# Optimization experiments

Hardware: AMD Instinct MI355X
Metric: run time of the kernel (lower is better)

The kernel has to match this reference:

```python
import jax, jax.numpy as jnp
import numpy as np

B, M, N, D, H = 8, 64, 64, 256, 8

def setup_inputs() -> dict:
    key = jax.random.key(0)
    kx, kq, kk, kv, ko = jax.random.split(key, 5)
    x = jax.random.normal(kx, (B, M, N, D), dtype=jnp.float32)
    q = jax.random.normal(kq, (H, D, D), dtype=jnp.float32)
    k = jax.random.normal(kk, (D, D), dtype=jnp.float32)
    v = jax.random.normal(kv, (D, D), dtype=jnp.float32)
    o = jax.random.normal(ko, (H, D, D), dtype=jnp.float32)
    return {"x": x, "q": q, "k": k, "v": v, "o": o}

def reference(x, q, k, v, o):
    # x: [b,m,n,d]; q,o: [h,d,d]; k,v: [d,d]
    Q = jnp.einsum('bmnd,hdk->bhmnk', x, q)      # [b,h,m,n,d]
    h_half = Q.shape[1] // 2
    Q1, Q2 = Q[:, :h_half], Q[:, h_half:]
    K = jnp.einsum('bmnd,dk->bmnk', x, k)        # [b,m,n,d]
    V = jnp.einsum('bmnd,dv->bmnv', x, v)        # [b,m,n,d]

    # Axis 1: attend along the m (row) axis for each column y
    logits1 = jnp.einsum('bhxyk,bzyk->bhyxz', Q1, K)   # [b,h/2,n,m,m]
    scores1 = jax.nn.softmax(logits1, axis=-1)
    O1 = jnp.einsum('bhyxz,bzyv->bhxyv', scores1, V)   # [b,h/2,m,n,d]

    # Axis 2: attend along the n (column) axis for each row x
    logits2 = jnp.einsum('bhxyk,bxzk->bhxyz', Q2, K)   # [b,h/2,m,n,n]
    scores2 = jax.nn.softmax(logits2, axis=-1)
    O2 = jnp.einsum('bhxyz,bxzv->bhxyv', scores2, V)   # [b,h/2,m,n,d]

    O = jnp.concatenate([O1, O2], axis=1)              # [b,h,m,n,d]
    # Faithful to original: 'bhmnd,hdv->bmnd' keeps d, sums over h and v
    Z = jnp.einsum('bhmnd,hdv->bmnd', O, o)
    return Z
```

## Files before the change

### kernel.cpp

```cpp
#include <hip/hip_runtime.h>

typedef unsigned short u16;
typedef __attribute__((ext_vector_type(8))) short short8;
typedef __attribute__((ext_vector_type(4))) float f32x4;

__device__ __forceinline__ float bf2f(u16 u){ return __uint_as_float(((unsigned)u)<<16); }
__device__ __forceinline__ u16 f2bf(float f){
  unsigned u = __float_as_uint(f);
  unsigned r = u + 0x7fffu + ((u>>16)&1u);
  return (u16)(r>>16);
}

#define MFMA16(a,b,c) __builtin_amdgcn_mfma_f32_16x16x32_bf16(a,b,c,0,0,0)

static constexpr int XS_STR  = 264;
static constexpr int PS_STR  = 72;
static constexpr int WT_STR  = 72;
static constexpr int XHI_OFF = 0;
static constexpr int XLO_OFF = 16896;
static constexpr int GT_OFF  = 33792;
static constexpr int XVT_OFF = 50688;
static constexpr int PS_OFF  = 69120;
static constexpr int SMRE_OFF= 73728;
static constexpr int SMEM_BYTES = (73728 + 512)*2;

static constexpr int MH_SMEM = 70656*2;


__global__ void prep_kernel(const float* __restrict__ k, const float* __restrict__ v,
                            const float* __restrict__ o, u16* __restrict__ khi,
                            u16* __restrict__ klo, u16* __restrict__ vT,
                            float* __restrict__ soP, float4* __restrict__ outz){
  __shared__ float Ts[64*65];
  const int blk = blockIdx.x, tid = threadIdx.x;
  if (blk < 64){
    int base = blk*1024 + tid*4;
    const float4 f4 = *(const float4*)(k + base);
    ushort4 hv, lv;
    hv.x=f2bf(f4.x); lv.x=f2bf(f4.x-bf2f(hv.x));
    hv.y=f2bf(f4.y); lv.y=f2bf(f4.y-bf2f(hv.y));
    hv.z=f2bf(f4.z); lv.z=f2bf(f4.z-bf2f(hv.z));
    hv.w=f2bf(f4.w); lv.w=f2bf(f4.w-bf2f(hv.w));
    *(ushort4*)&khi[base] = hv;
    *(ushort4*)&klo[base] = lv;
  } else if (blk < 80){
    int t = blk - 64;
    const int bi = (t>>2)<<6, bj = (t&3)<<6;
    #pragma unroll
    for (int p=0;p<4;p++){
      int idx4 = tid + (p<<8);
      int i = idx4 >> 4, c4 = (idx4 & 15) << 2;
      const float4 f4 = *(const float4*)(v + ((bi+i)<<8) + bj + c4);
      Ts[i*65+c4]=f4.x; Ts[i*65+c4+1]=f4.y; Ts[i*65+c4+2]=f4.z; Ts[i*65+c4+3]=f4.w;
    }
    __syncthreads();
    #pragma unroll
    for (int p=0;p<2;p++){
      int ch = tid + (p<<8);
      int j = ch >> 3, i8 = (ch & 7) << 3;
      short8 t8;
      #pragma unroll
      for (int e=0;e<8;e++) t8[e] = (short)f2bf(Ts[(i8+e)*65 + j]);
      *(short8*)&vT[((bj+j)<<8) + bi + i8] = t8;
    }
  } else if (blk < 336){
    int p = blk - 80;
    int h = p >> 5, base = (p & 31) << 3;
    int w = tid >> 6, l = tid & 63;
    #pragma unroll
    for (int i=0;i<2;i++){
      int row = base + w*2 + i;
      const float4 f4 = *(const float4*)(o + (((h<<8)+row)<<8) + (l<<2));
      float s = f4.x + f4.y + f4.z + f4.w;
      #pragma unroll
      for (int off=32; off>=1; off>>=1) s += __shfl_xor(s, off, 64);
      if (l==0) soP[(h<<8)+row] = s;
    }
  } else {
    int z = blk - 336;
    const float4 zf4 = {0.f,0.f,0.f,0.f};
    #pragma unroll
    for (int i=0;i<16;i++) outz[z*4096 + i*256 + tid] = zf4;
  }
}

__global__ __launch_bounds__(256,1) void mh_kernel(
    const float* __restrict__ q, const u16* __restrict__ khi,
    const u16* __restrict__ klo, u16* __restrict__ mhi, u16* __restrict__ mlo)
{
  extern __shared__ u16 sm[];
  u16* Qhi = sm;
  u16* Qlo = sm + 16896;
  u16* Chi = sm + 33792;
  u16* Clo = sm + 52224;

  const int tid = threadIdx.x;
  const int w = tid >> 6, lane = tid & 63;
  const int quad = lane >> 4, m16 = lane & 15;
  const int cw = w << 6, koq = quad << 3;
  const int h = blockIdx.x >> 2, dt = (blockIdx.x & 3) << 6;

  #pragma unroll
  for (int i=0;i<16;i++){
    int idx4 = i*256 + tid;
    int tr = idx4 >> 6, c4 = (idx4 & 63) << 2;
    const float4 xv = *(const float4*)(q + (((h<<8)+dt+tr)<<8) + c4);
    ushort4 hv, lv;
    hv.x=f2bf(xv.x); lv.x=f2bf(xv.x-bf2f(hv.x));
    hv.y=f2bf(xv.y); lv.y=f2bf(xv.y-bf2f(hv.y));
    hv.z=f2bf(xv.z); lv.z=f2bf(xv.z-bf2f(hv.z));
    hv.w=f2bf(xv.w); lv.w=f2bf(xv.w-bf2f(hv.w));
    *(ushort4*)&Qhi[tr*XS_STR + c4] = hv;
    *(ushort4*)&Qlo[tr*XS_STR + c4] = lv;
  }
  __syncthreads();

  const f32x4 zf = {0.f,0.f,0.f,0.f};
  f32x4 acc[4][4];
  #pragma unroll
  for (int r=0;r<4;r++)
    #pragma unroll
    for (int c=0;c<4;c++) acc[r][c] = zf;

  short8 Bh[2][4], Bl[2][4];
  #pragma unroll
  for (int c=0;c<4;c++){
    Bh[0][c] = *(const short8*)&khi[(cw + c*16 + m16)*256 + koq];
    Bl[0][c] = *(const short8*)&klo[(cw + c*16 + m16)*256 + koq];
  }
  #pragma unroll
  for (int kk=0;kk<8;kk++){
    const int cur = kk&1, nxt = cur^1;
    if (kk<7){
      const int ko2 = ((kk+1)<<5) + koq;
      #pragma unroll
      for (int c=0;c<4;c++){
        Bh[nxt][c] = *(const short8*)&khi[(cw + c*16 + m16)*256 + ko2];
        Bl[nxt][c] = *(const short8*)&klo[(cw + c*16 + m16)*256 + ko2];
      }
    }
    const int ko = (kk<<5) + koq;
    short8 Ah[4], Al[4];
    #pragma unroll
    for (int r=0;r<4;r++) Ah[r] = *(const short8*)&Qhi[(r*16+m16)*XS_STR + ko];
    #pragma unroll
    for (int r=0;r<4;r++) Al[r] = *(const short8*)&Qlo[(r*16+m16)*XS_STR + ko];
    #pragma unroll
    for (int r=0;r<4;r++)
      #pragma unroll
      for (int c=0;c<4;c++){
        acc[r][c] = MFMA16(Ah[r], Bh[cur][c], acc[r][c]);
        acc[r][c] = MFMA16(Ah[r], Bl[cur][c], acc[r][c]);
        acc[r][c] = MFMA16(Al[r], Bh[cur][c], acc[r][c]);
      }
  }

  #pragma unroll
  for (int r=0;r<4;r++)
    #pragma unroll
    for (int c=0;c<4;c++)
      #pragma unroll
      for (int g=0; g<4; g++){
        int drow = r*16 + quad*4 + g;
        int dp   = cw + c*16 + m16;
        float vv = acc[r][c][g];
        u16 hh = f2bf(vv);
        Chi[dp*WT_STR + drow] = hh;
        Clo[dp*WT_STR + drow] = f2bf(vv - bf2f(hh));
      }
  __syncthreads();

  #pragma unroll
  for (int p=0;p<8;p++){
    int ch = tid + (p<<8);
    int dp = ch >> 3, i8 = (ch & 7) << 3;
    *(int4*)&mhi[(((h<<8)+dp)<<8) + dt + i8] = *(const int4*)&Chi[dp*WT_STR + i8];
    *(int4*)&mlo[(((h<<8)+dp)<<8) + dt + i8] = *(const int4*)&Clo[dp*WT_STR + i8];
  }
}

__global__ __launch_bounds__(512,2) void attn_kernel(
    const float* __restrict__ x, const u16* __restrict__ mhiP,
    const u16* __restrict__ mloP, const u16* __restrict__ vT,
    const float* __restrict__ soP, float* __restrict__ out)
{
  extern __shared__ u16 sm[];
  u16* Xhi = sm + XHI_OFF;
  u16* Xlo = sm + XLO_OFF;
  u16* Gt  = sm + GT_OFF;
  u16* Xvt = sm + XVT_OFF;
  u16* Ps  = sm + PS_OFF;
  float* SMf = (float*)(sm + SMRE_OFF);

  const int tid  = threadIdx.x;
  const int w    = tid >> 6, lane = tid & 63;
  const int quad = lane >> 4, m16 = lane & 15;
  const int br   = blockIdx.x >> 9;
  const int idx  = blockIdx.x & 511;
  const int b    = idx >> 6, s = idx & 63;
  const int cw   = w << 5;
  const int rs   = (w >> 1) << 4;
  const int zh   = w & 1;
  const int koq  = quad << 3;

  auto tok = [&](int t)->int {
    int m = br ? s : t;
    int n = br ? t : s;
    return (((b<<6) + m) << 14) + (n << 8);
  };

  #pragma unroll
  for (int i=0;i<8;i++){
    int idx4 = i*512 + tid;
    int tr = idx4 >> 6, c4 = (idx4 & 63) << 2;
    const float4 xv = *(const float4*)(x + tok(tr) + c4);
    ushort4 hv, lv;
    hv.x=f2bf(xv.x); lv.x=f2bf(xv.x-bf2f(hv.x));
    hv.y=f2bf(xv.y); lv.y=f2bf(xv.y-bf2f(hv.y));
    hv.z=f2bf(xv.z); lv.z=f2bf(xv.z-bf2f(hv.z));
    hv.w=f2bf(xv.w); lv.w=f2bf(xv.w-bf2f(hv.w));
    *(ushort4*)&Xhi[tr*XS_STR + c4] = hv;
    *(ushort4*)&Xlo[tr*XS_STR + c4] = lv;
  }
  __syncthreads();

  short8 XB[16];
  #pragma unroll
  for (int kk=0;kk<8;kk++)
    #pragma unroll
    for (int c=0;c<2;c++)
      XB[kk*2+c] = *(const short8*)&Xhi[((zh<<5) + c*16 + m16)*XS_STR + (kk<<5) + koq];

  const f32x4 zf = {0.f,0.f,0.f,0.f};
  f32x4 acc[4][2];

  auto mm3 = [&](const u16* __restrict__ Whi, const u16* __restrict__ Wlo){
    #pragma unroll
    for (int r=0;r<4;r++){ acc[r][0] = zf; acc[r][1] = zf; }
    short8 Bh[2][2], Bl[2][2];
    #pragma unroll
    for (int c=0;c<2;c++){
      Bh[0][c] = *(const short8*)&Whi[(cw + c*16 + m16)*256 + koq];
      Bl[0][c] = *(const short8*)&Wlo[(cw + c*16 + m16)*256 + koq];
    }
    #pragma unroll
    for (int kk=0;kk<8;kk++){
      const int cur = kk&1, nxt = cur^1;
      if (kk<7){
        const int ko2 = ((kk+1)<<5) + koq;
        #pragma unroll
        for (int c=0;c<2;c++){
          Bh[nxt][c] = *(const short8*)&Whi[(cw + c*16 + m16)*256 + ko2];
          Bl[nxt][c] = *(const short8*)&Wlo[(cw + c*16 + m16)*256 + ko2];
        }
      }
      const int ko = (kk<<5) + koq;
      short8 Ah[4], Al[4];
      #pragma unroll
      for (int r=0;r<4;r++) Ah[r] = *(const short8*)&Xhi[(r*16+m16)*XS_STR + ko];
      #pragma unroll
      for (int r=0;r<4;r++) Al[r] = *(const short8*)&Xlo[(r*16+m16)*XS_STR + ko];
      #pragma unroll
      for (int r=0;r<4;r++)
        #pragma unroll
        for (int c=0;c<2;c++){
          acc[r][c] = MFMA16(Ah[r], Bh[cur][c], acc[r][c]);
          acc[r][c] = MFMA16(Ah[r], Bl[cur][c], acc[r][c]);
          acc[r][c] = MFMA16(Al[r], Bh[cur][c], acc[r][c]);
        }
    }
  };

  {
    #pragma unroll
    for (int r=0;r<4;r++){ acc[r][0] = zf; acc[r][1] = zf; }
    #pragma unroll
    for (int kk=0;kk<8;kk++){
      const int ko = (kk<<5) + koq;
      short8 A[4], Bf[2];
      #pragma unroll
      for (int r=0;r<4;r++) A[r]  = *(const short8*)&Xhi[(r*16+m16)*XS_STR + ko];
      #pragma unroll
      for (int c=0;c<2;c++) Bf[c] = *(const short8*)&vT[(cw + c*16 + m16)*256 + ko];
      #pragma unroll
      for (int r=0;r<4;r++)
        #pragma unroll
        for (int c=0;c<2;c++) acc[r][c] = MFMA16(A[r], Bf[c], acc[r][c]);
    }
    #pragma unroll
    for (int r=0;r<4;r++)
      #pragma unroll
      for (int c=0;c<2;c++)
        #pragma unroll
        for (int g=0; g<4; g++){
          int z  = r*16 + quad*4 + g;
          int vc = cw + c*16 + m16;
          Xvt[vc*WT_STR + z] = f2bf(acc[r][c][g]);
        }
  }

  f32x4 Z[4][2];
  #pragma unroll
  for (int r=0;r<4;r++){ Z[r][0] = zf; Z[r][1] = zf; }

  for (int h=0; h<4; h++){
    const int gh = br*4 + h;

    mm3(mhiP + gh*65536, mloP + gh*65536);
    #pragma unroll
    for (int r=0;r<4;r++)
      #pragma unroll
      for (int c=0;c<2;c++)
        #pragma unroll
        for (int g=0; g<4; g++){
          int row = r*16 + quad*4 + g;
          int col = cw + c*16 + m16;
          Gt[row*XS_STR + col] = f2bf(acc[r][c][g]);
        }
    __syncthreads();

    f32x4 L[2];
    L[0] = zf; L[1] = zf;
    #pragma unroll
    for (int kk=0;kk<8;kk++){
      const int ko = (kk<<5) + koq;
      short8 A = *(const short8*)&Gt[(rs+m16)*XS_STR + ko];
      #pragma unroll
      for (int c=0;c<2;c++){
        L[c] = MFMA16(A, XB[kk*2+c], L[c]);
        short8 Bl = *(const short8*)&Xlo[((zh<<5) + c*16 + m16)*XS_STR + ko];
        L[c] = MFMA16(A, Bl, L[c]);
      }
    }
    __syncthreads();
    #pragma unroll
    for (int r=0;r<4;r++)
      #pragma unroll
      for (int c=0;c<2;c++)
        #pragma unroll
        for (int g=0; g<4; g++){
          int row = r*16 + quad*4 + g;
          int col = cw + c*16 + m16;
          float vv = acc[r][c][g];
          u16 hh = f2bf(vv);
          Gt[row*XS_STR + col] = f2bf(vv - bf2f(hh));
        }
    __syncthreads();

    #pragma unroll
    for (int kk=0;kk<8;kk++){
      const int ko = (kk<<5) + koq;
      short8 A = *(const short8*)&Gt[(rs+m16)*XS_STR + ko];
      #pragma unroll
      for (int c=0;c<2;c++)
        L[c] = MFMA16(A, XB[kk*2+c], L[c]);
    }

    float mxl[4], sml[4];
    #pragma unroll
    for (int g=0; g<4; g++){
      float mx = fmaxf(L[0][g], L[1][g]);
      #pragma unroll
      for (int off=1; off<16; off<<=1) mx = fmaxf(mx, __shfl_xor(mx, off, 64));
      float sum = 0.f;
      #pragma unroll
      for (int c=0;c<2;c++){ float e = __expf(L[c][g]-mx); L[c][g] = e; sum += e; }
      #pragma unroll
      for (int off=1; off<16; off<<=1) sum += __shfl_xor(sum, off, 64);
      mxl[g] = mx; sml[g] = sum;
      if (m16 == 0){
        int row = rs + quad*4 + g;
        SMf[row*4 + zh*2]     = mx;
        SMf[row*4 + zh*2 + 1] = sum;
      }
    }
    __syncthreads();
    #pragma unroll
    for (int g=0; g<4; g++){
      int row = rs + quad*4 + g;
      float mxo = SMf[row*4 + (zh^1)*2];
      float smo = SMf[row*4 + (zh^1)*2 + 1];
      float M   = fmaxf(mxl[g], mxo);
      float al  = __expf(mxl[g]-M), ao = __expf(mxo-M);
      float scale = al / (sml[g]*al + smo*ao);
      #pragma unroll
      for (int c=0;c<2;c++)
        Ps[row*PS_STR + (zh<<5) + c*16 + m16] = f2bf(L[c][g]*scale);
    }
    __syncthreads();

    #pragma unroll
    for (int r=0;r<4;r++){ acc[r][0] = zf; acc[r][1] = zf; }
    #pragma unroll
    for (int kk=0;kk<2;kk++){
      const int ko = (kk<<5) + koq;
      short8 A[4], Bf[2];
      #pragma unroll
      for (int r=0;r<4;r++) A[r]  = *(const short8*)&Ps[(r*16+m16)*PS_STR + ko];
      #pragma unroll
      for (int c=0;c<2;c++) Bf[c] = *(const short8*)&Xvt[(cw + c*16 + m16)*WT_STR + ko];
      #pragma unroll
      for (int r=0;r<4;r++)
        #pragma unroll
        for (int c=0;c<2;c++) acc[r][c] = MFMA16(A[r], Bf[c], acc[r][c]);
    }
    float sc[2];
    sc[0] = soP[gh*256 + cw + m16];
    sc[1] = soP[gh*256 + cw + 16 + m16];
    #pragma unroll
    for (int r=0;r<4;r++)
      #pragma unroll
      for (int c=0;c<2;c++)
        #pragma unroll
        for (int g=0; g<4; g++) Z[r][c][g] += sc[c]*acc[r][c][g];
  }

  #pragma unroll
  for (int r=0;r<4;r++)
    #pragma unroll
    for (int c=0;c<2;c++)
      #pragma unroll
      for (int g=0; g<4; g++){
        int t   = r*16 + quad*4 + g;
        int col = cw + c*16 + m16;
        atomicAdd(&out[tok(t) + col], Z[r][c][g]);
      }
}

extern "C" void kernel_launch(void* const* d_in, const int* in_sizes, int n_in,
                              void* d_out, int out_size, void* d_ws, size_t ws_size,
                              hipStream_t stream) {
  const float* x = (const float*)d_in[0];
  const float* q = (const float*)d_in[1];
  const float* k = (const float*)d_in[2];
  const float* v = (const float*)d_in[3];
  const float* o = (const float*)d_in[4];
  u16* ws   = (u16*)d_ws;
  u16* mhi  = ws;
  u16* mlo  = ws + 524288;
  u16* khi  = ws + 1048576;
  u16* klo  = ws + 1114112;
  u16* vT   = ws + 1179648;
  float* soP = (float*)(ws + 1245184);
  float* out = (float*)d_out;

  prep_kernel<<<848, 256, 0, stream>>>(k, v, o, khi, klo, vT, soP, (float4*)d_out);
  (void)hipFuncSetAttribute(reinterpret_cast<const void*>(&mh_kernel),
                            hipFuncAttributeMaxDynamicSharedMemorySize, MH_SMEM);
  mh_kernel<<<32, 256, MH_SMEM, stream>>>(q, khi, klo, mhi, mlo);

  (void)hipFuncSetAttribute(reinterpret_cast<const void*>(&attn_kernel),
                            hipFuncAttributeMaxDynamicSharedMemorySize, SMEM_BYTES);
  attn_kernel<<<1024, 512, SMEM_BYTES, stream>>>(x, mhi, mlo, vT, soP, out);
}
```

Measured before the change: 341.4 us.

## Use 1024-thread attention blocks and split mh kernel into smaller tiles

Measured after the change: 374.1 us. 9.6% more time.

```diff
diff --git a/kernel.cpp b/kernel.cpp
--- a/kernel.cpp
+++ b/kernel.cpp
@@ -22,9 +22,11 @@
 static constexpr int XVT_OFF = 50688;
 static constexpr int PS_OFF  = 69120;
 static constexpr int SMRE_OFF= 73728;
-static constexpr int SMEM_BYTES = (73728 + 512)*2;
-
-static constexpr int MH_SMEM = 70656*2;
+static constexpr int SMEM_BYTES = (73728 + 1024)*2;
+
+static constexpr int MQ_STR  = 264;
+static constexpr int MC_STR  = 40;
+static constexpr int MH_SMEM = (8448*2 + 10240*2)*2;
 
 
 __global__ void prep_kernel(const float* __restrict__ k, const float* __restrict__ v,
@@ -90,18 +92,18 @@
 {
   extern __shared__ u16 sm[];
   u16* Qhi = sm;
-  u16* Qlo = sm + 16896;
-  u16* Chi = sm + 33792;
-  u16* Clo = sm + 52224;
+  u16* Qlo = sm + 8448;
+  u16* Chi = sm + 16896;
+  u16* Clo = sm + 27136;
 
   const int tid = threadIdx.x;
   const int w = tid >> 6, lane = tid & 63;
   const int quad = lane >> 4, m16 = lane & 15;
   const int cw = w << 6, koq = quad << 3;
-  const int h = blockIdx.x >> 2, dt = (blockIdx.x & 3) << 6;
-
-  #pragma unroll
-  for (int i=0;i<16;i++){
+  const int h = blockIdx.x >> 3, dt = (blockIdx.x & 7) << 5;
+
+  #pragma unroll
+  for (int i=0;i<8;i++){
     int idx4 = i*256 + tid;
     int tr = idx4 >> 6, c4 = (idx4 & 63) << 2;
     const float4 xv = *(const float4*)(q + (((h<<8)+dt+tr)<<8) + c4);
@@ -110,15 +112,15 @@
     hv.y=f2bf(xv.y); lv.y=f2bf(xv.y-bf2f(hv.y));
     hv.z=f2bf(xv.z); lv.z=f2bf(xv.z-bf2f(hv.z));
     hv.w=f2bf(xv.w); lv.w=f2bf(xv.w-bf2f(hv.w));
-    *(ushort4*)&Qhi[tr*XS_STR + c4] = hv;
-    *(ushort4*)&Qlo[tr*XS_STR + c4] = lv;
+    *(ushort4*)&Qhi[tr*MQ_STR + c4] = hv;
+    *(ushort4*)&Qlo[tr*MQ_STR + c4] = lv;
   }
   __syncthreads();
 
   const f32x4 zf = {0.f,0.f,0.f,0.f};
-  f32x4 acc[4][4];
-  #pragma unroll
-  for (int r=0;r<4;r++)
+  f32x4 acc[2][4];
+  #pragma unroll
+  for (int r=0;r<2;r++)
     #pragma unroll
     for (int c=0;c<4;c++) acc[r][c] = zf;
 
@@ -140,13 +142,14 @@
       }
     }
     const int ko = (kk<<5) + koq;
-    short8 Ah[4], Al[4];
-    #pragma unroll
-    for (int r=0;r<4;r++) Ah[r] = *(const short8*)&Qhi[(r*16+m16)*XS_STR + ko];
-    #pragma unroll
-    for (int r=0;r<4;r++) Al[r] = *(const short8*)&Qlo[(r*16+m16)*XS_STR + ko];
-    #pragma unroll
-    for (int r=0;r<4;r++)
+    short8 Ah[2], Al[2];
+    #pragma unroll
+    for (int r=0;r<2;r++){
+      Ah[r] = *(const short8*)&Qhi[(r*16+m16)*MQ_STR + ko];
+      Al[r] = *(const short8*)&Qlo[(r*16+m16)*MQ_STR + ko];
+    }
+    #pragma unroll
+    for (int r=0;r<2;r++)
       #pragma unroll
       for (int c=0;c<4;c++){
         acc[r][c] = MFMA16(Ah[r], Bh[cur][c], acc[r][c]);
@@ -156,30 +159,32 @@
   }
 
   #pragma unroll
-  for (int r=0;r<4;r++)
-    #pragma unroll
-    for (int c=0;c<4;c++)
-      #pragma unroll
-      for (int g=0; g<4; g++){
-        int drow = r*16 + quad*4 + g;
-        int dp   = cw + c*16 + m16;
-        float vv = acc[r][c][g];
-        u16 hh = f2bf(vv);
-        Chi[dp*WT_STR + drow] = hh;
-        Clo[dp*WT_STR + drow] = f2bf(vv - bf2f(hh));
-      }
+  for (int r=0;r<2;r++)
+    #pragma unroll
+    for (int c=0;c<4;c++){
+      int dp = cw + c*16 + m16;
+      int z0 = r*16 + quad*4;
+      ushort4 hv, lv;
+      float v0=acc[r][c][0], v1=acc[r][c][1], v2=acc[r][c][2], v3=acc[r][c][3];
+      hv.x=f2bf(v0); lv.x=f2bf(v0-bf2f(hv.x));
+      hv.y=f2bf(v1); lv.y=f2bf(v1-bf2f(hv.y));
+      hv.z=f2bf(v2); lv.z=f2bf(v2-bf2f(hv.z));
+      hv.w=f2bf(v3); lv.w=f2bf(v3-bf2f(hv.w));
+      *(ushort4*)&Chi[dp*MC_STR + z0] = hv;
+      *(ushort4*)&Clo[dp*MC_STR + z0] = lv;
+    }
   __syncthreads();
 
   #pragma unroll
-  for (int p=0;p<8;p++){
+  for (int p=0;p<4;p++){
     int ch = tid + (p<<8);
-    int dp = ch >> 3, i8 = (ch & 7) << 3;
-    *(int4*)&mhi[(((h<<8)+dp)<<8) + dt + i8] = *(const int4*)&Chi[dp*WT_STR + i8];
-    *(int4*)&mlo[(((h<<8)+dp)<<8) + dt + i8] = *(const int4*)&Clo[dp*WT_STR + i8];
+    int dp = ch >> 2, i8 = (ch & 3) << 3;
+    *(int4*)&mhi[((((h<<8)+dp)<<8)) + dt + i8] = *(const int4*)&Chi[dp*MC_STR + i8];
+    *(int4*)&mlo[((((h<<8)+dp)<<8)) + dt + i8] = *(const int4*)&Clo[dp*MC_STR + i8];
   }
 }
 
-__global__ __launch_bounds__(512,2) void attn_kernel(
+__global__ __launch_bounds__(1024,1) void attn_kernel(
     const float* __restrict__ x, const u16* __restrict__ mhiP,
     const u16* __restrict__ mloP, const u16* __restrict__ vT,
     const float* __restrict__ soP, float* __restrict__ out)
@@ -198,9 +203,10 @@
   const int br   = blockIdx.x >> 9;
   const int idx  = blockIdx.x & 511;
   const int b    = idx >> 6, s = idx & 63;
-  const int cw   = w << 5;
-  const int rs   = (w >> 1) << 4;
-  const int zh   = w & 1;
+  const int cc   = w << 4;
+  const int rs   = (w >> 2) << 4;
+  const int zq   = w & 3;
+  const int zb   = zq << 4;
   const int koq  = quad << 3;
 
   auto tok = [&](int t)->int {
@@ -210,8 +216,8 @@
   };
 
   #pragma unroll
-  for (int i=0;i<8;i++){
-    int idx4 = i*512 + tid;
+  for (int i=0;i<4;i++){
+    int idx4 = i*1024 + tid;
     int tr = idx4 >> 6, c4 = (idx4 & 63) << 2;
     const float4 xv = *(const float4*)(x + tok(tr) + c4);
     ushort4 hv, lv;
@@ -224,207 +230,166 @@
   }
   __syncthreads();
 
-  short8 XB[16];
-  #pragma unroll
-  for (int kk=0;kk<8;kk++)
-    #pragma unroll
-    for (int c=0;c<2;c++)
-      XB[kk*2+c] = *(const short8*)&Xhi[((zh<<5) + c*16 + m16)*XS_STR + (kk<<5) + koq];
-
   const f32x4 zf = {0.f,0.f,0.f,0.f};
-  f32x4 acc[4][2];
+  f32x4 acc[4];
 
   auto mm3 = [&](const u16* __restrict__ Whi, const u16* __restrict__ Wlo){
     #pragma unroll
-    for (int r=0;r<4;r++){ acc[r][0] = zf; acc[r][1] = zf; }
-    short8 Bh[2][2], Bl[2][2];
-    #pragma unroll
-    for (int c=0;c<2;c++){
-      Bh[0][c] = *(const short8*)&Whi[(cw + c*16 + m16)*256 + koq];
-      Bl[0][c] = *(const short8*)&Wlo[(cw + c*16 + m16)*256 + koq];
-    }
+    for (int r=0;r<4;r++) acc[r] = zf;
+    short8 Bh[2], Bl[2];
+    Bh[0] = *(const short8*)&Whi[(cc + m16)*256 + koq];
+    Bl[0] = *(const short8*)&Wlo[(cc + m16)*256 + koq];
     #pragma unroll
     for (int kk=0;kk<8;kk++){
       const int cur = kk&1, nxt = cur^1;
       if (kk<7){
         const int ko2 = ((kk+1)<<5) + koq;
-        #pragma unroll
-        for (int c=0;c<2;c++){
-          Bh[nxt][c] = *(const short8*)&Whi[(cw + c*16 + m16)*256 + ko2];
-          Bl[nxt][c] = *(const short8*)&Wlo[(cw + c*16 + m16)*256 + ko2];
-        }
+        Bh[nxt] = *(const short8*)&Whi[(cc + m16)*256 + ko2];
+        Bl[nxt] = *(const short8*)&Wlo[(cc + m16)*256 + ko2];
       }
       const int ko = (kk<<5) + koq;
-      short8 Ah[4], Al[4];
-      #pragma unroll
-      for (int r=0;r<4;r++) Ah[r] = *(const short8*)&Xhi[(r*16+m16)*XS_STR + ko];
-      #pragma unroll
-      for (int r=0;r<4;r++) Al[r] = *(const short8*)&Xlo[(r*16+m16)*XS_STR + ko];
-      #pragma unroll
-      for (int r=0;r<4;r++)
-        #pragma unroll
-        for (int c=0;c<2;c++){
-          acc[r][c] = MFMA16(Ah[r], Bh[cur][c], acc[r][c]);
-          acc[r][c] = MFMA16(Ah[r], Bl[cur][c], acc[r][c]);
-          acc[r][c] = MFMA16(Al[r], Bh[cur][c], acc[r][c]);
-        }
+      #pragma unroll
+      for (int r=0;r<4;r++){
+        short8 Ah = *(const short8*)&Xhi[(r*16+m16)*XS_STR + ko];
+        short8 Al = *(const short8*)&Xlo[(r*16+m16)*XS_STR + ko];
+        acc[r] = MFMA16(Ah, Bh[cur], acc[r]);
+        acc[r] = MFMA16(Ah, Bl[cur], acc[r]);
+        acc[r] = MFMA16(Al, Bh[cur], acc[r]);
+      }
     }
   };
 
   {
     #pragma unroll
-    for (int r=0;r<4;r++){ acc[r][0] = zf; acc[r][1] = zf; }
+    for (int r=0;r<4;r++) acc[r] = zf;
+    short8 Bv[2];
+    Bv[0] = *(const short8*)&vT[(cc + m16)*256 + koq];
+    #pragma unroll
+    for (int kk=0;kk<8;kk++){
+      const int cur = kk&1, nxt = cur^1;
+      if (kk<7)
+        Bv[nxt] = *(const short8*)&vT[(cc + m16)*256 + ((kk+1)<<5) + koq];
+      const int ko = (kk<<5) + koq;
+      #pragma unroll
+      for (int r=0;r<4;r++){
+        short8 Ah = *(const short8*)&Xhi[(r*16+m16)*XS_STR + ko];
+        acc[r] = MFMA16(Ah, Bv[cur], acc[r]);
+      }
+    }
+    #pragma unroll
+    for (int r=0;r<4;r++){
+      int vc = cc + m16;
+      int z0 = r*16 + quad*4;
+      ushort4 hv;
+      hv.x=f2bf(acc[r][0]); hv.y=f2bf(acc[r][1]);
+      hv.z=f2bf(acc[r][2]); hv.w=f2bf(acc[r][3]);
+      *(ushort4*)&Xvt[vc*WT_STR + z0] = hv;
+    }
+  }
+
+  f32x4 Z[4];
+  #pragma unroll
+  for (int r=0;r<4;r++) Z[r] = zf;
+
+  for (int h=0; h<4; h++){
+    const int gh = br*4 + h;
+
+    mm3(mhiP + gh*65536, mloP + gh*65536);
+    #pragma unroll
+    for (int r=0;r<4;r++)
+      #pragma unroll
+      for (int g=0; g<4; g++)
+        Gt[(r*16 + quad*4 + g)*XS_STR + cc + m16] = f2bf(acc[r][g]);
+    __syncthreads();
+
+    f32x4 L = zf;
     #pragma unroll
     for (int kk=0;kk<8;kk++){
       const int ko = (kk<<5) + koq;
-      short8 A[4], Bf[2];
-      #pragma unroll
-      for (int r=0;r<4;r++) A[r]  = *(const short8*)&Xhi[(r*16+m16)*XS_STR + ko];
-      #pragma unroll
-      for (int c=0;c<2;c++) Bf[c] = *(const short8*)&vT[(cw + c*16 + m16)*256 + ko];
-      #pragma unroll
-      for (int r=0;r<4;r++)
-        #pragma unroll
-        for (int c=0;c<2;c++) acc[r][c] = MFMA16(A[r], Bf[c], acc[r][c]);
-    }
+      short8 A  = *(const short8*)&Gt[(rs+m16)*XS_STR + ko];
+      short8 Bh = *(const short8*)&Xhi[(zb + m16)*XS_STR + ko];
+      short8 Bl = *(const short8*)&Xlo[(zb + m16)*XS_STR + ko];
+      L = MFMA16(A, Bh, L);
+      L = MFMA16(A, Bl, L);
+    }
+    __syncthreads();
     #pragma unroll
     for (int r=0;r<4;r++)
       #pragma unroll
-      for (int c=0;c<2;c++)
-        #pragma unroll
-        for (int g=0; g<4; g++){
-          int z  = r*16 + quad*4 + g;
-          int vc = cw + c*16 + m16;
-          Xvt[vc*WT_STR + z] = f2bf(acc[r][c][g]);
-        }
-  }
-
-  f32x4 Z[4][2];
-  #pragma unroll
-  for (int r=0;r<4;r++){ Z[r][0] = zf; Z[r][1] = zf; }
-
-  for (int h=0; h<4; h++){
-    const int gh = br*4 + h;
-
-    mm3(mhiP + gh*65536, mloP + gh*65536);
-    #pragma unroll
-    for (int r=0;r<4;r++)
-      #pragma unroll
-      for (int c=0;c<2;c++)
-        #pragma unroll
-        for (int g=0; g<4; g++){
-          int row = r*16 + quad*4 + g;
-          int col = cw + c*16 + m16;
-          Gt[row*XS_STR + col] = f2bf(acc[r][c][g]);
-        }
-    __syncthreads();
-
-    f32x4 L[2];
-    L[0] = zf; L[1] = zf;
+      for (int g=0; g<4; g++){
+        float vv = acc[r][g];
+        u16 hh = f2bf(vv);
+        Gt[(r*16 + quad*4 + g)*XS_STR + cc + m16] = f2bf(vv - bf2f(hh));
+      }
+    __syncthreads();
+
     #pragma unroll
     for (int kk=0;kk<8;kk++){
       const int ko = (kk<<5) + koq;
-      short8 A = *(const short8*)&Gt[(rs+m16)*XS_STR + ko];
-      #pragma unroll
-      for (int c=0;c<2;c++){
-        L[c] = MFMA16(A, XB[kk*2+c], L[c]);
-        short8 Bl = *(const short8*)&Xlo[((zh<<5) + c*16 + m16)*XS_STR + ko];
-        L[c] = MFMA16(A, Bl, L[c]);
-      }
-    }
-    __syncthreads();
-    #pragma unroll
-    for (int r=0;r<4;r++)
-      #pragma unroll
-      for (int c=0;c<2;c++)
-        #pragma unroll
-        for (int g=0; g<4; g++){
-          int row = r*16 + quad*4 + g;
-          int col = cw + c*16 + m16;
-          float vv = acc[r][c][g];
-          u16 hh = f2bf(vv);
-          Gt[row*XS_STR + col] = f2bf(vv - bf2f(hh));
-        }
-    __syncthreads();
-
-    #pragma unroll
-    for (int kk=0;kk<8;kk++){
-      const int ko = (kk<<5) + koq;
-      short8 A = *(const short8*)&Gt[(rs+m16)*XS_STR + ko];
-      #pragma unroll
-      for (int c=0;c<2;c++)
-        L[c] = MFMA16(A, XB[kk*2+c], L[c]);
+      short8 A  = *(const short8*)&Gt[(rs+m16)*XS_STR + ko];
+      short8 Bh = *(const short8*)&Xhi[(zb + m16)*XS_STR + ko];
+      L = MFMA16(A, Bh, L);
     }
 
     float mxl[4], sml[4];
     #pragma unroll
     for (int g=0; g<4; g++){
-      float mx = fmaxf(L[0][g], L[1][g]);
+      float mx = L[g];
       #pragma unroll
       for (int off=1; off<16; off<<=1) mx = fmaxf(mx, __shfl_xor(mx, off, 64));
-      float sum = 0.f;
-      #pragma unroll
-      for (int c=0;c<2;c++){ float e = __expf(L[c][g]-mx); L[c][g] = e; sum += e; }
+      float e = __expf(L[g]-mx);
+      float sum = e;
       #pragma unroll
       for (int off=1; off<16; off<<=1) sum += __shfl_xor(sum, off, 64);
-      mxl[g] = mx; sml[g] = sum;
+      L[g] = e; mxl[g] = mx; sml[g] = sum;
       if (m16 == 0){
         int row = rs + quad*4 + g;
-        SMf[row*4 + zh*2]     = mx;
-        SMf[row*4 + zh*2 + 1] = sum;
+        SMf[row*8 + zq*2]     = mx;
+        SMf[row*8 + zq*2 + 1] = sum;
       }
     }
     __syncthreads();
     #pragma unroll
     for (int g=0; g<4; g++){
       int row = rs + quad*4 + g;
-      float mxo = SMf[row*4 + (zh^1)*2];
-      float smo = SMf[row*4 + (zh^1)*2 + 1];
-      float M   = fmaxf(mxl[g], mxo);
-      float al  = __expf(mxl[g]-M), ao = __expf(mxo-M);
-      float scale = al / (sml[g]*al + smo*ao);
-      #pragma unroll
-      for (int c=0;c<2;c++)
-        Ps[row*PS_STR + (zh<<5) + c*16 + m16] = f2bf(L[c][g]*scale);
-    }
-    __syncthreads();
-
-    #pragma unroll
-    for (int r=0;r<4;r++){ acc[r][0] = zf; acc[r][1] = zf; }
+      float m0 = SMf[row*8+0], s0 = SMf[row*8+1];
+      float m1 = SMf[row*8+2], s1 = SMf[row*8+3];
+      float m2 = SMf[row*8+4], s2 = SMf[row*8+5];
+      float m3 = SMf[row*8+6], s3 = SMf[row*8+7];
+      float M  = fmaxf(fmaxf(m0,m1), fmaxf(m2,m3));
+      float den = s0*__expf(m0-M) + s1*__expf(m1-M)
+                + s2*__expf(m2-M) + s3*__expf(m3-M);
+      float scale = __expf(mxl[g]-M) / den;
+      Ps[row*PS_STR + zb + m16] = f2bf(L[g]*scale);
+    }
+    __syncthreads();
+
+    #pragma unroll
+    for (int r=0;r<4;r++) acc[r] = zf;
     #pragma unroll
     for (int kk=0;kk<2;kk++){
       const int ko = (kk<<5) + koq;
-      short8 A[4], Bf[2];
-      #pragma unroll
-      for (int r=0;r<4;r++) A[r]  = *(const short8*)&Ps[(r*16+m16)*PS_STR + ko];
-      #pragma unroll
-      for (int c=0;c<2;c++) Bf[c] = *(const short8*)&Xvt[(cw + c*16 + m16)*WT_STR + ko];
-      #pragma unroll
-      for (int r=0;r<4;r++)
-        #pragma unroll
-        for (int c=0;c<2;c++) acc[r][c] = MFMA16(A[r], Bf[c], acc[r][c]);
-    }
-    float sc[2];
-    sc[0] = soP[gh*256 + cw + m16];
-    sc[1] = soP[gh*256 + cw + 16 + m16];
+      short8 Bf = *(const short8*)&Xvt[(cc + m16)*WT_STR + ko];
+      #pragma unroll
+      for (int r=0;r<4;r++){
+        short8 A = *(const short8*)&Ps[(r*16+m16)*PS_STR + ko];
+        acc[r] = MFMA16(A, Bf, acc[r]);
+      }
+    }
+    float sc = soP[gh*256 + cc + m16];
     #pragma unroll
     for (int r=0;r<4;r++)
       #pragma unroll
-      for (int c=0;c<2;c++)
-        #pragma unroll
-        for (int g=0; g<4; g++) Z[r][c][g] += sc[c]*acc[r][c][g];
+      for (int g=0; g<4; g++) Z[r][g] += sc*acc[r][g];
   }
 
   #pragma unroll
   for (int r=0;r<4;r++)
     #pragma unroll
-    for (int c=0;c<2;c++)
-      #pragma unroll
-      for (int g=0; g<4; g++){
-        int t   = r*16 + quad*4 + g;
-        int col = cw + c*16 + m16;
-        atomicAdd(&out[tok(t) + col], Z[r][c][g]);
-      }
+    for (int g=0; g<4; g++){
+      int t = r*16 + quad*4 + g;
+      atomicAdd(&out[tok(t) + cc + m16], Z[r][g]);
+    }
 }
 
 extern "C" void kernel_launch(void* const* d_in, const int* in_sizes, int n_in,
@@ -447,9 +412,9 @@
   prep_kernel<<<848, 256, 0, stream>>>(k, v, o, khi, klo, vT, soP, (float4*)d_out);
   (void)hipFuncSetAttribute(reinterpret_cast<const void*>(&mh_kernel),
                             hipFuncAttributeMaxDynamicSharedMemorySize, MH_SMEM);
-  mh_kernel<<<32, 256, MH_SMEM, stream>>>(q, khi, klo, mhi, mlo);
+  mh_kernel<<<64, 256, MH_SMEM, stream>>>(q, khi, klo, mhi, mlo);
 
   (void)hipFuncSetAttribute(reinterpret_cast<const void*>(&attn_kernel),
                             hipFuncAttributeMaxDynamicSharedMemorySize, SMEM_BYTES);
-  attn_kernel<<<1024, 512, SMEM_BYTES, stream>>>(x, mhi, mlo, vT, soP, out);
+  attn_kernel<<<1024, 1024, SMEM_BYTES, stream>>>(x, mhi, mlo, vT, soP, out);
 }
```
